# Optimization experiments

Measured on AMD Instinct MI355X. Metric: run time of the kernel, lower is better.

Reference implementation:

```python
import jax, jax.numpy as jnp
import numpy as np

N_ROWS = 262144
FEAT = 1024
N_CORES = 4096
SEG = N_ROWS // N_CORES
H1 = H2 = H3 = 1024
NUM_CLASSES = 2
BN_EPS = 1e-5


def setup_inputs() -> dict:
    key = jax.random.key(0)
    ks = jax.random.split(key, 12)
    x = jax.random.normal(ks[0], (N_ROWS, FEAT), dtype=jnp.float32)
    # equal-length segments: start indices 0, SEG, 2*SEG, ...
    corelen = (jnp.arange(N_CORES) * SEG).astype(jnp.int64)
    def lin(k, din, dout):
        kw, kb = jax.random.split(k)
        W = jax.random.normal(kw, (din, dout), dtype=jnp.float32) / np.sqrt(din)
        b = jnp.zeros((dout,), dtype=jnp.float32)
        return W, b
    W1, b1 = lin(ks[1], FEAT, H1)
    W2, b2 = lin(ks[2], H1, H2)
    W3, b3 = lin(ks[3], H2, H3)
    W4, b4 = lin(ks[4], H3, NUM_CLASSES)
    g1 = jnp.ones((H1,), jnp.float32); be1 = jnp.zeros((H1,), jnp.float32)
    g2 = jnp.ones((H2,), jnp.float32); be2 = jnp.zeros((H2,), jnp.float32)
    g3 = jnp.ones((H3,), jnp.float32); be3 = jnp.zeros((H3,), jnp.float32)
    return {"x": x, "corelen": corelen,
            "W1": W1, "b1": b1, "g1": g1, "be1": be1,
            "W2": W2, "b2": b2, "g2": g2, "be2": be2,
            "W3": W3, "b3": b3, "g3": g3, "be3": be3,
            "W4": W4, "b4": b4}


def _batchnorm(h, g, b):
    # BatchNorm1d, training mode: biased batch statistics over the batch dim
    m = jnp.mean(h, axis=0)
    v = jnp.mean(jnp.square(h - m), axis=0)
    return g * (h - m) * jax.lax.rsqrt(v + BN_EPS) + b


def reference(x, corelen, W1, b1, g1, be1, W2, b2, g2, be2, W3, b3, g3, be3, W4, b4):
    n = x.shape[0]
    # segment id of row r = number of starts <= r, minus 1 (rows before
    # corelen[0] get id -1 and are dropped, matching the torch loop)
    seg_ids = jnp.searchsorted(corelen, jnp.arange(n), side="right") - 1
    agg = jax.ops.segment_sum(x, seg_ids, num_segments=corelen.shape[0])  # [C, FEAT]
    h = jax.nn.relu(_batchnorm(agg @ W1 + b1, g1, be1))
    h = jax.nn.relu(_batchnorm(h @ W2 + b2, g2, be2))
    h = jax.nn.relu(_batchnorm(h @ W3 + b3, g3, be3))
    return h @ W4 + b4  # [C, NUM_CLASSES]
```

## Files before the change

### kernel.cpp

```cpp
#include <hip/hip_runtime.h>
#include <hip/hip_bf16.h>
#include <stdint.h>

#define N_ROWS 262144
#define FEAT 1024
#define N_CORES 4096
#define HDIM 1024
#define BN_EPS 1e-5f

typedef __attribute__((ext_vector_type(8))) short bf16x8;
typedef __attribute__((ext_vector_type(8))) unsigned short u16x8;
typedef __attribute__((ext_vector_type(4))) float f32x4;

__device__ __forceinline__ unsigned short f2bf(float f) {
  __hip_bfloat16 h = __float2bfloat16(f);
  return __builtin_bit_cast(unsigned short, h);
}
__device__ __forceinline__ float bf2f(unsigned short u) {
  unsigned int x = ((unsigned int)u) << 16;
  return __builtin_bit_cast(float, x);
}

__device__ __forceinline__ void gll16(const unsigned short* g, unsigned short* l) {
  __builtin_amdgcn_global_load_lds(
      (const __attribute__((address_space(1))) void*)g,
      (__attribute__((address_space(3))) void*)l, 16, 0, 0);
}

__global__ __launch_bounds__(256)
void k_segsum(const float* __restrict__ x, const int* __restrict__ corelen,
              unsigned short* __restrict__ aggb) {
  const int seg = blockIdx.x;
  const int t = threadIdx.x;
  const int start = corelen[seg];
  const int end = (seg + 1 < N_CORES) ? corelen[seg + 1] : N_ROWS;
  f32x4 a0 = {0.f, 0.f, 0.f, 0.f};
  f32x4 a1 = {0.f, 0.f, 0.f, 0.f};
  f32x4 a2 = {0.f, 0.f, 0.f, 0.f};
  f32x4 a3 = {0.f, 0.f, 0.f, 0.f};
  const f32x4* xp = (const f32x4*)(x + (size_t)start * FEAT) + t;
  int r = start;
  for (; r + 4 <= end; r += 4) {
    const f32x4 v0 = __builtin_nontemporal_load(xp);
    const f32x4 v1 = __builtin_nontemporal_load(xp + 256);
    const f32x4 v2 = __builtin_nontemporal_load(xp + 512);
    const f32x4 v3 = __builtin_nontemporal_load(xp + 768);
    a0 += v0; a1 += v1; a2 += v2; a3 += v3;
    xp += 4 * 256;
  }
  for (; r < end; ++r) {
    a0 += *xp;
    xp += 256;
  }
  a0 += a1; a2 += a3; a0 += a2;
  ushort4 o;
  o.x = f2bf(a0.x); o.y = f2bf(a0.y); o.z = f2bf(a0.z); o.w = f2bf(a0.w);
  *(ushort4*)(aggb + (size_t)seg * FEAT + t * 4) = o;
}

__global__ __launch_bounds__(256)
void k_transpose_all(const float* __restrict__ W1, const float* __restrict__ W2,
                     const float* __restrict__ W3, unsigned short* __restrict__ Wt) {
  __shared__ unsigned short tile[32][33];
  const int l = blockIdx.z;
  const float* W = (l == 0) ? W1 : (l == 1) ? W2 : W3;
  unsigned short* Wo = Wt + (size_t)l * HDIM * HDIM;
  const int tx = threadIdx.x, ty = threadIdx.y;
  const int n0 = blockIdx.x * 32, k0 = blockIdx.y * 32;
#pragma unroll
  for (int i = 0; i < 4; ++i)
    tile[ty + 8 * i][tx] = f2bf(W[(size_t)(k0 + ty + 8 * i) * HDIM + n0 + tx]);
  __syncthreads();
#pragma unroll
  for (int i = 0; i < 4; ++i)
    Wo[(size_t)(n0 + ty + 8 * i) * HDIM + k0 + tx] = tile[tx][ty + 8 * i];
}

#define BM 64
#define BN 64
#define BK 64
#define NT (HDIM / BK)
__global__ __launch_bounds__(64)
void k_gemm_bt(const unsigned short* __restrict__ A,
               const unsigned short* __restrict__ Bt,
               const float* __restrict__ bias,
               unsigned short* __restrict__ C,
               float* __restrict__ sums, float* __restrict__ sumsq) {
  __shared__ unsigned short As[2][BM * BK];
  __shared__ unsigned short Bs[2][BN * BK];
  const int lane = threadIdx.x;
  const int tileM = blockIdx.x * BM;
  const int tileN = blockIdx.y * BN;
  const int fr = lane & 15;
  const int kk = (lane >> 4) * 8;
  const int lr = lane >> 3;
  const int sc = ((lane & 7) * 8) ^ (lr << 3);

  const unsigned short* pA = A + (size_t)(tileM + lr) * HDIM + sc;
  const unsigned short* pB = Bt + (size_t)(tileN + lr) * HDIM + sc;

  f32x4 acc[4][4] = {};

#define STAGE(buf, k0)                                                     \
  do {                                                                     \
    _Pragma("unroll") for (int j = 0; j < 8; ++j)                          \
        gll16(pA + (k0) + j * 8 * HDIM, &As[buf][(j * 8) * BK]);           \
    _Pragma("unroll") for (int j = 0; j < 8; ++j)                          \
        gll16(pB + (k0) + j * 8 * HDIM, &Bs[buf][(j * 8) * BK]);           \
  } while (0)

  STAGE(0, 0);
  STAGE(1, BK);
  for (int kt = 0; kt < NT; ++kt) {
    const int cur = kt & 1;
    if (kt < NT - 1)
      asm volatile("s_waitcnt vmcnt(16)" ::: "memory");
    else
      asm volatile("s_waitcnt vmcnt(0)" ::: "memory");
    __builtin_amdgcn_sched_barrier(0);
    bf16x8 af[2][4], bfv[2][4];
#pragma unroll
    for (int ks = 0; ks < 2; ++ks) {
      const int pc = (ks * 32 + kk) ^ ((fr & 7) << 3);
#pragma unroll
      for (int m = 0; m < 4; ++m)
        af[ks][m] = *(const bf16x8*)&As[cur][(m * 16 + fr) * BK + pc];
#pragma unroll
      for (int n = 0; n < 4; ++n)
        bfv[ks][n] = *(const bf16x8*)&Bs[cur][(n * 16 + fr) * BK + pc];
    }
    asm volatile("s_waitcnt lgkmcnt(0)" ::: "memory");
    __builtin_amdgcn_sched_barrier(0);
    if (kt + 2 < NT) STAGE(cur, (kt + 2) * BK);
#pragma unroll
    for (int ks = 0; ks < 2; ++ks)
#pragma unroll
      for (int m = 0; m < 4; ++m)
#pragma unroll
        for (int n = 0; n < 4; ++n)
          acc[m][n] = __builtin_amdgcn_mfma_f32_16x16x32_bf16(
              af[ks][m], bfv[ks][n], acc[m][n], 0, 0, 0);
  }
#undef STAGE

  const int cr = (lane >> 4) * 4;
  const int cc = lane & 15;
#pragma unroll
  for (int n = 0; n < 4; ++n) {
    const int col = tileN + n * 16 + cc;
    const float bv = bias[col];
    float s = 0.f, s2 = 0.f;
#pragma unroll
    for (int m = 0; m < 4; ++m) {
      unsigned short* cp = C + (size_t)(tileM + m * 16 + cr) * HDIM + col;
#pragma unroll
      for (int j = 0; j < 4; ++j) {
        const float h = acc[m][n][j] + bv;
        cp[(size_t)j * HDIM] = f2bf(h);
        s += h; s2 += h * h;
      }
    }
    s  += __shfl_xor(s, 16, 64);  s  += __shfl_xor(s, 32, 64);
    s2 += __shfl_xor(s2, 16, 64); s2 += __shfl_xor(s2, 32, 64);
    if ((lane >> 4) == 0) {
      atomicAdd(&sums[col], s);
      atomicAdd(&sumsq[col], s2);
    }
  }
}

__global__ __launch_bounds__(256)
void k_norm_relu(const unsigned short* __restrict__ Hb,
                 const float* __restrict__ sums, const float* __restrict__ sumsq,
                 const float* __restrict__ g, const float* __restrict__ be,
                 unsigned short* __restrict__ Ab) {
  const size_t i8 = ((size_t)blockIdx.x * 256 + threadIdx.x) * 8;
  const u16x8 v = *(const u16x8*)(Hb + i8);
  const int c = (int)(i8 & (HDIM - 1));
  u16x8 o;
#pragma unroll
  for (int j = 0; j < 8; ++j) {
    const float mean = sums[c + j] * (1.f / N_CORES);
    const float var = sumsq[c + j] * (1.f / N_CORES) - mean * mean;
    const float sc = g[c + j] * rsqrtf(var + BN_EPS);
    const float sh = be[c + j] - mean * sc;
    o[j] = f2bf(fmaxf(bf2f(v[j]) * sc + sh, 0.f));
  }
  *(u16x8*)(Ab + i8) = o;
}

__global__ __launch_bounds__(256)
void k_final(const unsigned short* __restrict__ Hb,
             const float* __restrict__ sums, const float* __restrict__ sumsq,
             const float* __restrict__ g, const float* __restrict__ be,
             const float* __restrict__ W4, const float* __restrict__ b4,
             float* __restrict__ out) {
  const int t = threadIdx.x;
  const int w = t >> 6, lane = t & 63;
  const int row = blockIdx.x * 4 + w;
  const int kbase = lane * 16;
  const unsigned short* a = Hb + (size_t)row * HDIM + kbase;
  float s0 = 0.f, s1 = 0.f;
#pragma unroll
  for (int j = 0; j < 16; ++j) {
    const int col = kbase + j;
    const float mean = sums[col] * (1.f / N_CORES);
    const float var = sumsq[col] * (1.f / N_CORES) - mean * mean;
    const float sc = g[col] * rsqrtf(var + BN_EPS);
    const float sh = be[col] - mean * sc;
    const float av = fmaxf(bf2f(a[j]) * sc + sh, 0.f);
    s0 += av * W4[col * 2 + 0];
    s1 += av * W4[col * 2 + 1];
  }
#pragma unroll
  for (int off = 32; off >= 1; off >>= 1) {
    s0 += __shfl_down(s0, off, 64);
    s1 += __shfl_down(s1, off, 64);
  }
  if (lane == 0) {
    out[row * 2 + 0] = s0 + b4[0];
    out[row * 2 + 1] = s1 + b4[1];
  }
}

extern "C" void kernel_launch(void* const* d_in, const int* in_sizes, int n_in,
                              void* d_out, int out_size, void* d_ws, size_t ws_size,
                              hipStream_t stream) {
  (void)in_sizes; (void)n_in; (void)out_size; (void)ws_size;
  const float* x       = (const float*)d_in[0];
  const int* corelen   = (const int*)d_in[1];
  const float* W1  = (const float*)d_in[2];
  const float* b1  = (const float*)d_in[3];
  const float* g1  = (const float*)d_in[4];
  const float* be1 = (const float*)d_in[5];
  const float* W2  = (const float*)d_in[6];
  const float* b2  = (const float*)d_in[7];
  const float* g2  = (const float*)d_in[8];
  const float* be2 = (const float*)d_in[9];
  const float* W3  = (const float*)d_in[10];
  const float* b3  = (const float*)d_in[11];
  const float* g3  = (const float*)d_in[12];
  const float* be3 = (const float*)d_in[13];
  const float* W4  = (const float*)d_in[14];
  const float* b4  = (const float*)d_in[15];
  float* out = (float*)d_out;

  char* ws = (char*)d_ws;
  unsigned short* Hb   = (unsigned short*)(ws);
  unsigned short* Abf  = (unsigned short*)(ws + (8u << 20));
  unsigned short* Wt   = (unsigned short*)(ws + (16u << 20));
  float* stats = (float*)(ws + (22u << 20));

  hipMemsetAsync(stats, 0, 6 * HDIM * sizeof(float), stream);
  k_transpose_all<<<dim3(32, 32, 3), dim3(32, 8), 0, stream>>>(W1, W2, W3, Wt);
  k_segsum<<<N_CORES, 256, 0, stream>>>(x, corelen, Abf);

  const float* bs[3]  = {b1, b2, b3};
  const float* gs[3]  = {g1, g2, g3};
  const float* bes[3] = {be1, be2, be3};
  for (int l = 0; l < 3; ++l) {
    float* sums  = stats + l * 2 * HDIM;
    float* sumsq = sums + HDIM;
    k_gemm_bt<<<dim3(N_CORES / BM, HDIM / BN), 64, 0, stream>>>(
        Abf, Wt + (size_t)l * HDIM * HDIM, bs[l], Hb, sums, sumsq);
    if (l < 2)
      k_norm_relu<<<(N_CORES * HDIM / 8) / 256, 256, 0, stream>>>(
          Hb, sums, sumsq, gs[l], bes[l], Abf);
    else
      k_final<<<N_CORES / 4, 256, 0, stream>>>(
          Hb, sums, sumsq, gs[l], bes[l], W4, b4, out);
  }
}
```

Baseline: 256.8 us.

## Fuse prep kernels into one launch and halve GEMM K-tile to 32

Merges the stats memset, the weight transpose/convert and the segment-sum into a single heterogeneous k_prep launch, with block-id ranges selecting the role. This removes two launches and lets the transpose blocks overlap with the bandwidth-bound segment sum. Separately, the GEMM K-tile drops from 64 to 32, which halves LDS per stage and the per-iteration loads, with the swizzle and vmcnt counts adjusted to match. The smaller tile lowers LDS use and may raise occupancy, but it doubles the loop iterations and syncs per MFMA.

```diff
diff --git a/kernel.cpp b/kernel.cpp
--- a/kernel.cpp
+++ b/kernel.cpp
@@ -28,57 +28,65 @@
 }
 
 __global__ __launch_bounds__(256)
-void k_segsum(const float* __restrict__ x, const int* __restrict__ corelen,
-              unsigned short* __restrict__ aggb) {
-  const int seg = blockIdx.x;
+void k_prep(const float* __restrict__ x, const int* __restrict__ corelen,
+            unsigned short* __restrict__ aggb,
+            const float* __restrict__ W1, const float* __restrict__ W2,
+            const float* __restrict__ W3, unsigned short* __restrict__ Wt,
+            float* __restrict__ stats) {
+  const int bid = blockIdx.x;
   const int t = threadIdx.x;
-  const int start = corelen[seg];
-  const int end = (seg + 1 < N_CORES) ? corelen[seg + 1] : N_ROWS;
-  f32x4 a0 = {0.f, 0.f, 0.f, 0.f};
-  f32x4 a1 = {0.f, 0.f, 0.f, 0.f};
-  f32x4 a2 = {0.f, 0.f, 0.f, 0.f};
-  f32x4 a3 = {0.f, 0.f, 0.f, 0.f};
-  const f32x4* xp = (const f32x4*)(x + (size_t)start * FEAT) + t;
-  int r = start;
-  for (; r + 4 <= end; r += 4) {
-    const f32x4 v0 = __builtin_nontemporal_load(xp);
-    const f32x4 v1 = __builtin_nontemporal_load(xp + 256);
-    const f32x4 v2 = __builtin_nontemporal_load(xp + 512);
-    const f32x4 v3 = __builtin_nontemporal_load(xp + 768);
-    a0 += v0; a1 += v1; a2 += v2; a3 += v3;
-    xp += 4 * 256;
-  }
-  for (; r < end; ++r) {
-    a0 += *xp;
-    xp += 256;
-  }
-  a0 += a1; a2 += a3; a0 += a2;
-  ushort4 o;
-  o.x = f2bf(a0.x); o.y = f2bf(a0.y); o.z = f2bf(a0.z); o.w = f2bf(a0.w);
-  *(ushort4*)(aggb + (size_t)seg * FEAT + t * 4) = o;
-}
-
-__global__ __launch_bounds__(256)
-void k_transpose_all(const float* __restrict__ W1, const float* __restrict__ W2,
-                     const float* __restrict__ W3, unsigned short* __restrict__ Wt) {
-  __shared__ unsigned short tile[32][33];
-  const int l = blockIdx.z;
-  const float* W = (l == 0) ? W1 : (l == 1) ? W2 : W3;
-  unsigned short* Wo = Wt + (size_t)l * HDIM * HDIM;
-  const int tx = threadIdx.x, ty = threadIdx.y;
-  const int n0 = blockIdx.x * 32, k0 = blockIdx.y * 32;
-#pragma unroll
-  for (int i = 0; i < 4; ++i)
-    tile[ty + 8 * i][tx] = f2bf(W[(size_t)(k0 + ty + 8 * i) * HDIM + n0 + tx]);
-  __syncthreads();
-#pragma unroll
-  for (int i = 0; i < 4; ++i)
-    Wo[(size_t)(n0 + ty + 8 * i) * HDIM + k0 + tx] = tile[tx][ty + 8 * i];
+  if (bid < N_CORES) {
+    const int seg = bid;
+    const int start = corelen[seg];
+    const int end = (seg + 1 < N_CORES) ? corelen[seg + 1] : N_ROWS;
+    f32x4 a0 = {0.f, 0.f, 0.f, 0.f};
+    f32x4 a1 = {0.f, 0.f, 0.f, 0.f};
+    f32x4 a2 = {0.f, 0.f, 0.f, 0.f};
+    f32x4 a3 = {0.f, 0.f, 0.f, 0.f};
+    const f32x4* xp = (const f32x4*)(x + (size_t)start * FEAT) + t;
+    int r = start;
+    for (; r + 4 <= end; r += 4) {
+      const f32x4 v0 = __builtin_nontemporal_load(xp);
+      const f32x4 v1 = __builtin_nontemporal_load(xp + 256);
+      const f32x4 v2 = __builtin_nontemporal_load(xp + 512);
+      const f32x4 v3 = __builtin_nontemporal_load(xp + 768);
+      a0 += v0; a1 += v1; a2 += v2; a3 += v3;
+      xp += 4 * 256;
+    }
+    for (; r < end; ++r) {
+      a0 += *xp;
+      xp += 256;
+    }
+    a0 += a1; a2 += a3; a0 += a2;
+    ushort4 o;
+    o.x = f2bf(a0.x); o.y = f2bf(a0.y); o.z = f2bf(a0.z); o.w = f2bf(a0.w);
+    *(ushort4*)(aggb + (size_t)seg * FEAT + t * 4) = o;
+  } else if (bid < N_CORES + 3 * 1024) {
+    __shared__ unsigned short tile[32][33];
+    const int id = bid - N_CORES;
+    const int l = id >> 10;
+    const int q = id & 1023;
+    const int n0 = (q & 31) * 32;
+    const int k0 = (q >> 5) * 32;
+    const float* W = (l == 0) ? W1 : (l == 1) ? W2 : W3;
+    unsigned short* Wo = Wt + (size_t)l * HDIM * HDIM;
+    const int tx = t & 31, ty = t >> 5;
+#pragma unroll
+    for (int i = 0; i < 4; ++i)
+      tile[ty + 8 * i][tx] = f2bf(W[(size_t)(k0 + ty + 8 * i) * HDIM + n0 + tx]);
+    __syncthreads();
+#pragma unroll
+    for (int i = 0; i < 4; ++i)
+      Wo[(size_t)(n0 + ty + 8 * i) * HDIM + k0 + tx] = tile[tx][ty + 8 * i];
+  } else {
+#pragma unroll
+    for (int i = 0; i < 24; ++i) stats[t + i * 256] = 0.f;
+  }
 }
 
 #define BM 64
 #define BN 64
-#define BK 64
+#define BK 32
 #define NT (HDIM / BK)
 __global__ __launch_bounds__(64)
 void k_gemm_bt(const unsigned short* __restrict__ A,
@@ -93,8 +101,8 @@
   const int tileN = blockIdx.y * BN;
   const int fr = lane & 15;
   const int kk = (lane >> 4) * 8;
-  const int lr = lane >> 3;
-  const int sc = ((lane & 7) * 8) ^ (lr << 3);
+  const int lr = lane >> 2;
+  const int sc = ((lane & 3) * 8) ^ ((lr & 3) * 8);
 
   const unsigned short* pA = A + (size_t)(tileM + lr) * HDIM + sc;
   const unsigned short* pB = Bt + (size_t)(tileN + lr) * HDIM + sc;
@@ -103,10 +111,10 @@
 
 #define STAGE(buf, k0)                                                     \
   do {                                                                     \
-    _Pragma("unroll") for (int j = 0; j < 8; ++j)                          \
-        gll16(pA + (k0) + j * 8 * HDIM, &As[buf][(j * 8) * BK]);           \
-    _Pragma("unroll") for (int j = 0; j < 8; ++j)                          \
-        gll16(pB + (k0) + j * 8 * HDIM, &Bs[buf][(j * 8) * BK]);           \
+    _Pragma("unroll") for (int j = 0; j < 4; ++j)                          \
+        gll16(pA + (k0) + j * 16 * HDIM, &As[buf][(j * 16) * BK]);         \
+    _Pragma("unroll") for (int j = 0; j < 4; ++j)                          \
+        gll16(pB + (k0) + j * 16 * HDIM, &Bs[buf][(j * 16) * BK]);         \
   } while (0)
 
   STAGE(0, 0);
@@ -114,32 +122,27 @@
   for (int kt = 0; kt < NT; ++kt) {
     const int cur = kt & 1;
     if (kt < NT - 1)
-      asm volatile("s_waitcnt vmcnt(16)" ::: "memory");
+      asm volatile("s_waitcnt vmcnt(8)" ::: "memory");
     else
       asm volatile("s_waitcnt vmcnt(0)" ::: "memory");
     __builtin_amdgcn_sched_barrier(0);
-    bf16x8 af[2][4], bfv[2][4];
-#pragma unroll
-    for (int ks = 0; ks < 2; ++ks) {
-      const int pc = (ks * 32 + kk) ^ ((fr & 7) << 3);
-#pragma unroll
-      for (int m = 0; m < 4; ++m)
-        af[ks][m] = *(const bf16x8*)&As[cur][(m * 16 + fr) * BK + pc];
-#pragma unroll
-      for (int n = 0; n < 4; ++n)
-        bfv[ks][n] = *(const bf16x8*)&Bs[cur][(n * 16 + fr) * BK + pc];
-    }
+    const int pc = kk ^ ((fr & 3) * 8);
+    bf16x8 af[4], bfv[4];
+#pragma unroll
+    for (int m = 0; m < 4; ++m)
+      af[m] = *(const bf16x8*)&As[cur][(m * 16 + fr) * BK + pc];
+#pragma unroll
+    for (int n = 0; n < 4; ++n)
+      bfv[n] = *(const bf16x8*)&Bs[cur][(n * 16 + fr) * BK + pc];
     asm volatile("s_waitcnt lgkmcnt(0)" ::: "memory");
     __builtin_amdgcn_sched_barrier(0);
     if (kt + 2 < NT) STAGE(cur, (kt + 2) * BK);
 #pragma unroll
-    for (int ks = 0; ks < 2; ++ks)
-#pragma unroll
-      for (int m = 0; m < 4; ++m)
-#pragma unroll
-        for (int n = 0; n < 4; ++n)
-          acc[m][n] = __builtin_amdgcn_mfma_f32_16x16x32_bf16(
-              af[ks][m], bfv[ks][n], acc[m][n], 0, 0, 0);
+    for (int m = 0; m < 4; ++m)
+#pragma unroll
+      for (int n = 0; n < 4; ++n)
+        acc[m][n] = __builtin_amdgcn_mfma_f32_16x16x32_bf16(
+            af[m], bfv[n], acc[m][n], 0, 0, 0);
   }
 #undef STAGE
 
@@ -251,9 +254,8 @@
   unsigned short* Wt   = (unsigned short*)(ws + (16u << 20));
   float* stats = (float*)(ws + (22u << 20));
 
-  hipMemsetAsync(stats, 0, 6 * HDIM * sizeof(float), stream);
-  k_transpose_all<<<dim3(32, 32, 3), dim3(32, 8), 0, stream>>>(W1, W2, W3, Wt);
-  k_segsum<<<N_CORES, 256, 0, stream>>>(x, corelen, Abf);
+  k_prep<<<N_CORES + 3 * 1024 + 1, 256, 0, stream>>>(
+      x, corelen, Abf, W1, W2, W3, Wt, stats);
 
   const float* bs[3]  = {b1, b2, b3};
   const float* gs[3]  = {g1, g2, g3};
```

Result: no change. 261.3 us (+1.7%).
